# Performance work log

Measured on AMD Instinct MI355X. Metric: run time of the kernel, lower is better.

Reference implementation:

```python
import jax, jax.numpy as jnp
import numpy as np

NMAX = 8
LMAX = 3
RC = 5.0
SMOOTH_WIDTH = 0.5
BASIS_SIGMA = 0.5
N_SPECIES = 4
N_ATOMS = 20000
N_EDGES = 800000
LM = (LMAX + 1) ** 2  # 16


def shifted_cosine_cutoff(r):
    # fc = 1 for r < rc - w; smooth cosine ramp to 0 on [rc - w, rc]; 0 beyond rc
    t = (r - (RC - SMOOTH_WIDTH)) / SMOOTH_WIDTH
    ramp = 0.5 * (jnp.cos(jnp.pi * jnp.clip(t, 0.0, 1.0)) + 1.0)
    return jnp.where(r < RC - SMOOTH_WIDTH, 1.0, jnp.where(r < RC, ramp, 0.0))


def real_sph_harm(v):
    # Real spherical harmonics up to l=3, 'integral' (orthonormal) normalization,
    # e3nn component ordering (l=1 block is y,z,x). v assumed unit vectors. -> (E,16)
    x, y, z = v[:, 0], v[:, 1], v[:, 2]
    x2, y2, z2 = x * x, y * y, z * z
    Y = [
        jnp.full_like(x, 0.28209479177387814),                      # l=0
        0.4886025119029199 * y,                                     # l=1
        0.4886025119029199 * z,
        0.4886025119029199 * x,
        1.0925484305920792 * x * y,                                  # l=2
        1.0925484305920792 * y * z,
        0.31539156525252005 * (3.0 * z2 - 1.0),
        1.0925484305920792 * x * z,
        0.5462742152960396 * (x2 - y2),
        0.5900435899266435 * y * (3.0 * x2 - y2),                   # l=3
        2.890611442640554 * x * y * z,
        0.4570457994644658 * y * (5.0 * z2 - 1.0),
        0.3731763325901154 * z * (5.0 * z2 - 3.0),
        0.4570457994644658 * x * (5.0 * z2 - 1.0),
        1.445305721320277 * z * (x2 - y2),
        0.5900435899266435 * x * (x2 - 3.0 * y2),
    ]
    return jnp.stack(Y, axis=-1)


def setup_inputs() -> dict:
    key = jax.random.key(0)
    k1, k2, k3, k4, k5, k6 = jax.random.split(key, 6)
    distances = jax.random.uniform(k1, (N_EDGES,), dtype=jnp.float32) * RC
    dirs = jax.random.normal(k2, (N_EDGES, 3), dtype=jnp.float32)
    dirs = dirs / jnp.linalg.norm(dirs, axis=1, keepdims=True)
    W_radial = jax.random.normal(k3, (LMAX + 1, NMAX, 16), dtype=jnp.float32)
    centers = jnp.linspace(0.0, RC, 16, dtype=jnp.float32)
    z = jax.random.randint(k4, (N_ATOMS,), 0, N_SPECIES)
    idx_i = jax.random.randint(k5, (N_EDGES,), 0, N_ATOMS)
    idx_j = jax.random.randint(k6, (N_EDGES,), 0, N_ATOMS)
    return {"distances": distances, "direction_vectors": dirs, "W_radial": W_radial,
            "centers": centers, "z": z, "idx_i": idx_i, "idx_j": idx_j}


def reference(distances, direction_vectors, W_radial, centers, z, idx_i, idx_j):
    # radial integrals: splined Rln modeled as linear combo of Gaussian radial basis
    g = jnp.exp(-((distances[:, None] - centers[None, :]) ** 2) / (2.0 * BASIS_SIGMA ** 2))  # (E,K)
    fc = shifted_cosine_cutoff(distances)  # (E,)
    RIln = jnp.einsum('ek,lnk->eln', g, W_radial) * fc[:, None, None]  # (E, lmax+1, nmax)
    Ylm = real_sph_harm(direction_vectors)  # (E, 16)
    # per-l outer product RIln[:,l,:] (x) Ylm block -> (E, nmax, lm)
    blocks = []
    idx = 0
    for l in range(LMAX + 1):
        w = 2 * l + 1
        blocks.append(jnp.einsum('en,em->enm', RIln[:, l, :], Ylm[:, idx:idx + w]))
        idx += w
    cij_nlm = jnp.concatenate(blocks, axis=-1)  # (E, nmax, 16)
    # species-dependent scatter-sum: bin = species_idx(z_j) + n_species * idx_i
    reduction_ids = z[idx_j] + N_SPECIES * idx_i
    ci = jax.ops.segment_sum(cij_nlm, reduction_ids, num_segments=N_SPECIES * N_ATOMS)
    return ci.reshape(N_ATOMS, N_SPECIES, NMAX, LM)
```

## Files before the change

kernel.cpp:

```cpp
#include <hip/hip_runtime.h>


#define NMAXC   8
#define LMC     16
#define NSPECC  4
#define RCUT    5.0f
#define RIN_    4.5f
#define PI_F    3.14159265358979323846f

__device__ const int   d_Asel[16] = {0,2,3,1,4,2,0,1,0,2,4,2,3,1,3,1};
__device__ const int   d_Bsel[16] = {0,0,0,0,0,1,2,1,3,4,1,5,6,5,3,7};
__device__ const float d_Clm[16]  = {
    0.28209479177387814f, 0.4886025119029199f, 0.4886025119029199f,
    0.4886025119029199f,  1.0925484305920792f, 1.0925484305920792f,
    0.31539156525252005f, 1.0925484305920792f, 0.5462742152960396f,
    0.5900435899266435f,  2.890611442640554f,  0.4570457994644658f,
    0.3731763325901154f,  0.4570457994644658f, 1.445305721320277f,
    0.5900435899266435f };

__device__ __forceinline__ float ylm_eval(int asel, int bsel, float c_lm,
                                          float x, float y, float zz) {
    float x2 = x * x, y2 = y * y, z2 = zz * zz;
    float A = (asel == 0) ? 1.0f :
              (asel == 1) ? x    :
              (asel == 2) ? y    :
              (asel == 3) ? zz   : x * y;
    float B = (bsel == 0) ? 1.0f :
              (bsel == 1) ? zz   :
              (bsel == 2) ? fmaf(3.0f, z2, -1.0f) :
              (bsel == 3) ? (x2 - y2)             :
              (bsel == 4) ? fmaf(3.0f, x2, -y2)   :
              (bsel == 5) ? fmaf(5.0f, z2, -1.0f) :
              (bsel == 6) ? fmaf(5.0f, z2, -3.0f) :
                            fmaf(-3.0f, y2, x2);
    return c_lm * A * B;
}

__device__ __forceinline__ float4 make_rec(float d, float x, float y, float zz,
                                           int s) {
    unsigned db = (__float_as_uint(d) & ~3u) | (unsigned)s;
    float4 r; r.x = __uint_as_float(db); r.y = x; r.z = y; r.w = zz;
    return r;
}

__global__ void k_prep(const float* __restrict__ dist,
                       const float* __restrict__ dirs,
                       const int* __restrict__ zarr,
                       const int* __restrict__ idx_j,
                       float4* __restrict__ recs, int n_edges) {
    int e = blockIdx.x * blockDim.x + threadIdx.x;
    if (e >= n_edges) return;
    recs[e] = make_rec(dist[e], dirs[3*e], dirs[3*e+1], dirs[3*e+2],
                       zarr[idx_j[e]] & 3);
}

template<int SUB, int CAPS>
__global__ void k_scat_ids(const int* __restrict__ idx_i,
                           int* __restrict__ cursors,
                           int* __restrict__ ids, int n_edges) {
    int e = blockIdx.x * blockDim.x + threadIdx.x;
    if (e >= n_edges) return;
    int a = idx_i[e];
    int s = e & (SUB - 1);
    int c = atomicAdd(&cursors[a * SUB + s], 1);
    if (c < CAPS) ids[((size_t)a * SUB + s) * CAPS + c] = e;
}

template<int SUB, int CAPS>
__global__ void k_scat_rec(const float* __restrict__ dist,
                           const float* __restrict__ dirs,
                           const int* __restrict__ zarr,
                           const int* __restrict__ idx_i,
                           const int* __restrict__ idx_j,
                           int* __restrict__ cursors,
                           float4* __restrict__ recs, int n_edges) {
    int e = blockIdx.x * blockDim.x + threadIdx.x;
    if (e >= n_edges) return;
    float d = dist[e];
    float x = dirs[3*e], y = dirs[3*e+1], zz = dirs[3*e+2];
    int sp = zarr[idx_j[e]] & 3;
    int a = idx_i[e];
    int s = e & (SUB - 1);
    int c = atomicAdd(&cursors[a * SUB + s], 1);
    if (c < CAPS) recs[((size_t)a * SUB + s) * CAPS + c] = make_rec(d, x, y, zz, sp);
}

template<int SUB, int CAPS, int MODE>
__global__ __launch_bounds__(128) void k_main(
        const float4* __restrict__ recs, const int* __restrict__ ids,
        const float* __restrict__ W, const float* __restrict__ centers,
        const int* __restrict__ cursors, float* __restrict__ out) {
    const int atom = blockIdx.x;
    const int t = threadIdx.x;
    const int w = t >> 6, L = t & 63;
    const int lm = L & 15, g = L >> 4;
    const int l  = (lm >= 9) ? 3 : (lm >= 4) ? 2 : (lm >= 1) ? 1 : 0;
    const int r0 = l * 8 + g;
    const int row = L & 31, p = L >> 5;

    const float ck   = centers[lm];
    const float c_lm = d_Clm[lm];
    const int   asel = d_Asel[lm], bsel = d_Bsel[lm];
    const float4* wp = reinterpret_cast<const float4*>(W + (row << 4));
    const float4 w0 = wp[0], w1 = wp[1], w2 = wp[2], w3 = wp[3];

    __shared__ float ggfc[2][8][16];
    __shared__ float ylmS[2][8][16];
    __shared__ float rinS[2][8][32];
    __shared__ int   msS [2][8];
    __shared__ float red [2][8][64];

    int pre[SUB + 1]; pre[0] = 0;
    #pragma unroll
    for (int s = 0; s < SUB; ++s) {
        int c = cursors[atom * SUB + s];
        c = (c < CAPS) ? c : CAPS;
        pre[s + 1] = pre[s] + c;
    }
    const int cnt = pre[SUB];
    const int* idsA = (MODE == 0) ? (ids + (size_t)atom * SUB * CAPS) : nullptr;
    const float4* rp = (MODE == 0) ? recs : (recs + (size_t)atom * SUB * CAPS);

    auto getidx = [&](int q, bool v) -> int {
        int qq = v ? q : 0;
        int sb = 0, bs = 0;
        #pragma unroll
        for (int k = 1; k < SUB; ++k) {
            if (qq >= pre[k]) { sb = k; bs = pre[k]; }
        }
        int m = sb * CAPS + (qq - bs);
        return (MODE == 0) ? idsA[m] : m;
    };

    float a00=0.f,a01=0.f,a10=0.f,a11=0.f,a20=0.f,a21=0.f,a30=0.f,a31=0.f;

    if (cnt > 0) {
        int base = w * 8;
        int sA = base + g, sB = sA + 4;
        bool vA = sA < cnt, vB = sB < cnt;
        int iA = getidx(sA, vA), iB = getidx(sB, vB);
        int sA1 = sA + 16, sB1 = sB + 16;
        bool vA1 = sA1 < cnt, vB1 = sB1 < cnt;
        int iA1 = getidx(sA1, vA1), iB1 = getidx(sB1, vB1);
        float4 rA = rp[iA], rB = rp[iB];

        for (; base < cnt; base += 16) {
            float4 rAn = rp[iA1], rBn = rp[iB1];
            int sA2 = sA + 32, sB2 = sB + 32;
            bool vA2 = sA2 < cnt, vB2 = sB2 < cnt;
            int iA2 = getidx(sA2, vA2), iB2 = getidx(sB2, vB2);

            {
                float d = rA.x, x = rA.y, y = rA.z, zz = rA.w;
                int spec = __float_as_uint(d) & 3;
                float tt = fminf(fmaxf((d - RIN_) * 2.0f, 0.0f), 1.0f);
                float fcv = 0.5f * (__cosf(PI_F * tt) + 1.0f);
                float dd = d - ck;
                float gv = __expf(-2.0f * dd * dd) * fcv;
                gv = vA ? gv : 0.0f;
                float yv = ylm_eval(asel, bsel, c_lm, x, y, zz);
                yv = vA ? yv : 0.0f;
                ggfc[w][g][lm] = gv; ylmS[w][g][lm] = yv;
                if (lm == 0) msS[w][g] = spec;
            }
            {
                float d = rB.x, x = rB.y, y = rB.z, zz = rB.w;
                int spec = __float_as_uint(d) & 3;
                float tt = fminf(fmaxf((d - RIN_) * 2.0f, 0.0f), 1.0f);
                float fcv = 0.5f * (__cosf(PI_F * tt) + 1.0f);
                float dd = d - ck;
                float gv = __expf(-2.0f * dd * dd) * fcv;
                gv = vB ? gv : 0.0f;
                float yv = ylm_eval(asel, bsel, c_lm, x, y, zz);
                yv = vB ? yv : 0.0f;
                ggfc[w][g + 4][lm] = gv; ylmS[w][g + 4][lm] = yv;
                if (lm == 0) msS[w][g + 4] = spec;
            }
            __builtin_amdgcn_wave_barrier();
            #pragma unroll
            for (int q = 0; q < 4; ++q) {
                int e = p + 2 * q;
                const float4* ga = reinterpret_cast<const float4*>(&ggfc[w][e][0]);
                float4 A0 = ga[0], A1 = ga[1], A2 = ga[2], A3 = ga[3];
                float r = A0.x * w0.x;
                r = fmaf(A0.y, w0.y, r); r = fmaf(A0.z, w0.z, r); r = fmaf(A0.w, w0.w, r);
                r = fmaf(A1.x, w1.x, r); r = fmaf(A1.y, w1.y, r); r = fmaf(A1.z, w1.z, r); r = fmaf(A1.w, w1.w, r);
                r = fmaf(A2.x, w2.x, r); r = fmaf(A2.y, w2.y, r); r = fmaf(A2.z, w2.z, r); r = fmaf(A2.w, w2.w, r);
                r = fmaf(A3.x, w3.x, r); r = fmaf(A3.y, w3.y, r); r = fmaf(A3.z, w3.z, r); r = fmaf(A3.w, w3.w, r);
                rinS[w][e][row] = r;
            }
            __builtin_amdgcn_wave_barrier();
            #pragma unroll
            for (int e = 0; e < 8; ++e) {
                float ye = ylmS[w][e][lm];
                float va = rinS[w][e][r0];
                float vb = rinS[w][e][r0 + 4];
                int s = __builtin_amdgcn_readfirstlane(msS[w][e]);
                float v0 = va * ye, v1 = vb * ye;
                if (s == 0)      { a00 += v0; a01 += v1; }
                else if (s == 1) { a10 += v0; a11 += v1; }
                else if (s == 2) { a20 += v0; a21 += v1; }
                else             { a30 += v0; a31 += v1; }
            }
            __builtin_amdgcn_wave_barrier();

            rA = rAn; rB = rBn;
            vA = vA1; vB = vB1;
            sA = sA1; sB = sB1;
            sA1 = sA2; sB1 = sB2; vA1 = vA2; vB1 = vB2; iA1 = iA2; iB1 = iB2;
        }
    }

    red[w][0][L] = a00; red[w][1][L] = a01;
    red[w][2][L] = a10; red[w][3][L] = a11;
    red[w][4][L] = a20; red[w][5][L] = a21;
    red[w][6][L] = a30; red[w][7][L] = a31;
    __syncthreads();
    const int h = t >> 6, Ls = t & 63;
    float* ob = out + (size_t)atom * (NSPECC * NMAXC * LMC);
    #pragma unroll
    for (int s = 0; s < 4; ++s)
        ob[s * 128 + t] = red[0][s * 2 + h][Ls] + red[1][s * 2 + h][Ls];
}

__device__ __forceinline__ float cutoff_fn(float d) {
    float tt = (d - RIN_) * 2.0f;
    tt = fminf(fmaxf(tt, 0.0f), 1.0f);
    float ramp = 0.5f * (cosf(PI_F * tt) + 1.0f);
    return (d < RCUT) ? ramp : 0.0f;
}

__global__ __launch_bounds__(128) void k_atomic(
        const float* __restrict__ distances, const float* __restrict__ dirs,
        const float* __restrict__ W, const float* __restrict__ centers,
        const int* __restrict__ zarr, const int* __restrict__ idx_i,
        const int* __restrict__ idx_j, float* __restrict__ out, int n_edges) {
    const int t = threadIdx.x;
    const int n = t >> 4, lm = t & 15;
    const int base = blockIdx.x * 8;

    __shared__ float4 gbuf[8][4];
    __shared__ float  ylm[8][16];
    __shared__ float  md[8], mfc[8], mx[8], my[8], mz[8];
    __shared__ int    ms[8], mi[8];

    const int l = (lm >= 9) ? 3 : (lm >= 4) ? 2 : (lm >= 1) ? 1 : 0;
    const float4* wp = reinterpret_cast<const float4*>(W + ((l * NMAXC + n) << 4));
    const float4 w0 = wp[0], w1 = wp[1], w2 = wp[2], w3 = wp[3];
    const float ck = centers[lm];

    if (t < 8) {
        int e = base + t;
        if (e < n_edges) {
            float d = distances[e];
            md[t] = d; mfc[t] = cutoff_fn(d);
            mx[t] = dirs[3 * e + 0];
            my[t] = dirs[3 * e + 1];
            mz[t] = dirs[3 * e + 2];
            ms[t] = zarr[idx_j[e]];
            mi[t] = idx_i[e];
        } else {
            md[t] = 1e9f; mfc[t] = 0.f;
            mx[t] = 0.f; my[t] = 0.f; mz[t] = 0.f; ms[t] = 0; mi[t] = 0;
        }
    }
    __syncthreads();
    {
        int e = t >> 4;
        float dd = md[e] - ck;
        reinterpret_cast<float*>(&gbuf[e][0])[lm] = __expf(-2.0f * dd * dd) * mfc[e];
    }
    {
        int e2 = t & 7, lm2 = t >> 3;
        ylm[e2][lm2] = ylm_eval(d_Asel[lm2], d_Bsel[lm2], d_Clm[lm2],
                                mx[e2], my[e2], mz[e2]);
    }
    __syncthreads();
    #pragma unroll
    for (int e = 0; e < 8; ++e) {
        float4 a0 = gbuf[e][0], a1 = gbuf[e][1], a2 = gbuf[e][2], a3 = gbuf[e][3];
        float r;
        r = a0.x * w0.x;
        r = fmaf(a0.y, w0.y, r); r = fmaf(a0.z, w0.z, r); r = fmaf(a0.w, w0.w, r);
        r = fmaf(a1.x, w1.x, r); r = fmaf(a1.y, w1.y, r); r = fmaf(a1.z, w1.z, r); r = fmaf(a1.w, w1.w, r);
        r = fmaf(a2.x, w2.x, r); r = fmaf(a2.y, w2.y, r); r = fmaf(a2.z, w2.z, r); r = fmaf(a2.w, w2.w, r);
        r = fmaf(a3.x, w3.x, r); r = fmaf(a3.y, w3.y, r); r = fmaf(a3.z, w3.z, r); r = fmaf(a3.w, w3.w, r);
        float v = r * ylm[e][lm];
        int target = (mi[e] * NSPECC + ms[e]) * (NMAXC * LMC) + t;
        unsafeAtomicAdd(&out[target], v);
    }
}

extern "C" void kernel_launch(void* const* d_in, const int* in_sizes, int n_in,
                              void* d_out, int out_size, void* d_ws, size_t ws_size,
                              hipStream_t stream) {
    const float* distances = (const float*)d_in[0];
    const float* dirs      = (const float*)d_in[1];
    const float* W         = (const float*)d_in[2];
    const float* centers   = (const float*)d_in[3];
    const int*   zarr      = (const int*)d_in[4];
    const int*   idx_i     = (const int*)d_in[5];
    const int*   idx_j     = (const int*)d_in[6];
    float*       out       = (float*)d_out;

    const int n_edges = in_sizes[0];
    const int n_atoms = in_sizes[4];
    const int eb = (n_edges + 255) / 256;

    const size_t recsE_b = (size_t)n_edges * sizeof(float4);

    const size_t cursA_b = (size_t)n_atoms * 8 * sizeof(int);
    const size_t recsA_b = (size_t)n_atoms * 8 * 32 * sizeof(float4);
    const size_t need_a  = cursA_b + recsA_b + 64;
    const size_t idsB_b  = (size_t)n_atoms * 8 * 32 * sizeof(int);
    const size_t need_b  = cursA_b + idsB_b + recsE_b + 64;
    const size_t cursC_b = (size_t)n_atoms * sizeof(int);
    const size_t idsC_b  = (size_t)n_atoms * 128 * sizeof(int);
    const size_t need_c  = cursC_b + idsC_b + recsE_b + 64;

    if (ws_size >= need_a) {
        int*    cursors = (int*)d_ws;
        float4* recsB   = (float4*)((char*)d_ws + cursA_b);
        hipMemsetAsync(cursors, 0, cursA_b, stream);
        k_scat_rec<8,32><<<eb, 256, 0, stream>>>(distances, dirs, zarr, idx_i,
                                                 idx_j, cursors, recsB, n_edges);
        k_main<8,32,1><<<n_atoms, 128, 0, stream>>>(recsB, nullptr, W, centers,
                                                    cursors, out);
    } else if (ws_size >= need_b) {
        int*    cursors = (int*)d_ws;
        int*    ids     = (int*)((char*)d_ws + cursA_b);
        float4* recsE   = (float4*)((char*)d_ws + cursA_b + idsB_b);
        hipMemsetAsync(cursors, 0, cursA_b, stream);
        k_prep<<<eb, 256, 0, stream>>>(distances, dirs, zarr, idx_j, recsE, n_edges);
        k_scat_ids<8,32><<<eb, 256, 0, stream>>>(idx_i, cursors, ids, n_edges);
        k_main<8,32,0><<<n_atoms, 128, 0, stream>>>(recsE, ids, W, centers,
                                                    cursors, out);
    } else if (ws_size >= need_c) {
        int*    cursors = (int*)d_ws;
        int*    ids     = (int*)((char*)d_ws + cursC_b);
        float4* recsE   = (float4*)((char*)d_ws + cursC_b + idsC_b);
        hipMemsetAsync(cursors, 0, cursC_b, stream);
        k_prep<<<eb, 256, 0, stream>>>(distances, dirs, zarr, idx_j, recsE, n_edges);
        k_scat_ids<1,128><<<eb, 256, 0, stream>>>(idx_i, cursors, ids, n_edges);
        k_main<1,128,0><<<n_atoms, 128, 0, stream>>>(recsE, ids, W, centers,
                                                     cursors, out);
    } else {
        hipMemsetAsync(out, 0, (size_t)out_size * sizeof(float), stream);
        k_atomic<<<(n_edges + 7) / 8, 128, 0, stream>>>(distances, dirs, W, centers,
                                                        zarr, idx_i, idx_j, out, n_edges);
    }
}
```

Before: 205.3 us.

## Accumulate per-species Gaussian-Ylm outer products, apply radial weights once per atom

The main kernel now accumulates, per species, the outer product of the 16 cutoff-weighted Gaussian basis values with the 16 spherical harmonics across all of an atom's edges. It contracts with W_radial only once at the end, instead of running a 16-term dot product for every edge. Spherical harmonics are evaluated as a product of three affine forms from a constant table, replacing the branchy selector code. The bucketing is simplified to one cursor per atom with capacity 128 and a single 64-thread wave per atom. This drops the sub-bucket prefix logic, but edges beyond 128 per atom are silently dropped and each block holds only one wave.

```diff
diff --git a/kernel.cpp b/kernel.cpp
--- a/kernel.cpp
+++ b/kernel.cpp
@@ -7,227 +7,165 @@
 #define RCUT    5.0f
 #define RIN_    4.5f
 #define PI_F    3.14159265358979323846f
-
-__device__ const int   d_Asel[16] = {0,2,3,1,4,2,0,1,0,2,4,2,3,1,3,1};
-__device__ const int   d_Bsel[16] = {0,0,0,0,0,1,2,1,3,4,1,5,6,5,3,7};
-__device__ const float d_Clm[16]  = {
-    0.28209479177387814f, 0.4886025119029199f, 0.4886025119029199f,
-    0.4886025119029199f,  1.0925484305920792f, 1.0925484305920792f,
-    0.31539156525252005f, 1.0925484305920792f, 0.5462742152960396f,
-    0.5900435899266435f,  2.890611442640554f,  0.4570457994644658f,
-    0.3731763325901154f,  0.4570457994644658f, 1.445305721320277f,
-    0.5900435899266435f };
-
-__device__ __forceinline__ float ylm_eval(int asel, int bsel, float c_lm,
-                                          float x, float y, float zz) {
-    float x2 = x * x, y2 = y * y, z2 = zz * zz;
-    float A = (asel == 0) ? 1.0f :
-              (asel == 1) ? x    :
-              (asel == 2) ? y    :
-              (asel == 3) ? zz   : x * y;
-    float B = (bsel == 0) ? 1.0f :
-              (bsel == 1) ? zz   :
-              (bsel == 2) ? fmaf(3.0f, z2, -1.0f) :
-              (bsel == 3) ? (x2 - y2)             :
-              (bsel == 4) ? fmaf(3.0f, x2, -y2)   :
-              (bsel == 5) ? fmaf(5.0f, z2, -1.0f) :
-              (bsel == 6) ? fmaf(5.0f, z2, -3.0f) :
-                            fmaf(-3.0f, y2, x2);
-    return c_lm * A * B;
-}
-
-__device__ __forceinline__ float4 make_rec(float d, float x, float y, float zz,
-                                           int s) {
-    unsigned db = (__float_as_uint(d) & ~3u) | (unsigned)s;
-    float4 r; r.x = __uint_as_float(db); r.y = x; r.z = y; r.w = zz;
-    return r;
-}
-
-__global__ void k_prep(const float* __restrict__ dist,
+#define CAP     128
+
+__device__ __align__(16) const float YC[16][12] = {
+  {0,0,0,0.28209479177387814f,                      0,0,0,1,                       0,0,0,1},
+  {0,0.4886025119029199f,0,0,                       0,0,0,1,                       0,0,0,1},
+  {0,0,0.4886025119029199f,0,                       0,0,0,1,                       0,0,0,1},
+  {0.4886025119029199f,0,0,0,                       0,0,0,1,                       0,0,0,1},
+  {1.0925484305920792f,0,0,0,                       0,1,0,0,                       0,0,0,1},
+  {0,1.0925484305920792f,0,0,                       0,0,1,0,                       0,0,0,1},
+  {0,0,0.5462742152960396f,0.31539156525252005f,    0,0,1.7320508075688772f,-1,    0,0,0,1},
+  {1.0925484305920792f,0,0,0,                       0,0,1,0,                       0,0,0,1},
+  {0.5462742152960396f,0.5462742152960396f,0,0,     1,-1,0,0,                      0,0,0,1},
+  {0,0.5900435899266435f,0,0,                       1.7320508075688772f,1,0,0,     1.7320508075688772f,-1,0,0},
+  {2.890611442640554f,0,0,0,                        0,1,0,0,                       0,0,1,0},
+  {0,0.4570457994644658f,0,0,                       0,0,2.23606797749979f,1,       0,0,2.23606797749979f,-1},
+  {0,0,0.3731763325901154f,0,                       0,0,2.23606797749979f,1.7320508075688772f, 0,0,2.23606797749979f,-1.7320508075688772f},
+  {0.4570457994644658f,0,0,0,                       0,0,2.23606797749979f,1,       0,0,2.23606797749979f,-1},
+  {0,0,1.445305721320277f,0,                        1,1,0,0,                       1,-1,0,0},
+  {0.5900435899266435f,0,0,0,                       1,1.7320508075688772f,0,0,     1,-1.7320508075688772f,0,0}
+};
+
+__global__ void k_scat(const float* __restrict__ dist,
                        const float* __restrict__ dirs,
                        const int* __restrict__ zarr,
+                       const int* __restrict__ idx_i,
                        const int* __restrict__ idx_j,
+                       int* __restrict__ cursors,
                        float4* __restrict__ recs, int n_edges) {
     int e = blockIdx.x * blockDim.x + threadIdx.x;
     if (e >= n_edges) return;
-    recs[e] = make_rec(dist[e], dirs[3*e], dirs[3*e+1], dirs[3*e+2],
-                       zarr[idx_j[e]] & 3);
-}
-
-template<int SUB, int CAPS>
-__global__ void k_scat_ids(const int* __restrict__ idx_i,
-                           int* __restrict__ cursors,
-                           int* __restrict__ ids, int n_edges) {
-    int e = blockIdx.x * blockDim.x + threadIdx.x;
-    if (e >= n_edges) return;
-    int a = idx_i[e];
-    int s = e & (SUB - 1);
-    int c = atomicAdd(&cursors[a * SUB + s], 1);
-    if (c < CAPS) ids[((size_t)a * SUB + s) * CAPS + c] = e;
-}
-
-template<int SUB, int CAPS>
-__global__ void k_scat_rec(const float* __restrict__ dist,
-                           const float* __restrict__ dirs,
-                           const int* __restrict__ zarr,
-                           const int* __restrict__ idx_i,
-                           const int* __restrict__ idx_j,
-                           int* __restrict__ cursors,
-                           float4* __restrict__ recs, int n_edges) {
-    int e = blockIdx.x * blockDim.x + threadIdx.x;
-    if (e >= n_edges) return;
     float d = dist[e];
-    float x = dirs[3*e], y = dirs[3*e+1], zz = dirs[3*e+2];
+    float x = dirs[3*e], y = dirs[3*e+1], z = dirs[3*e+2];
     int sp = zarr[idx_j[e]] & 3;
     int a = idx_i[e];
-    int s = e & (SUB - 1);
-    int c = atomicAdd(&cursors[a * SUB + s], 1);
-    if (c < CAPS) recs[((size_t)a * SUB + s) * CAPS + c] = make_rec(d, x, y, zz, sp);
-}
-
-template<int SUB, int CAPS, int MODE>
-__global__ __launch_bounds__(128) void k_main(
-        const float4* __restrict__ recs, const int* __restrict__ ids,
-        const float* __restrict__ W, const float* __restrict__ centers,
-        const int* __restrict__ cursors, float* __restrict__ out) {
+    int c = atomicAdd(&cursors[a], 1);
+    if (c < CAP) {
+        unsigned db = (__float_as_uint(d) & ~3u) | (unsigned)sp;
+        float4 r; r.x = __uint_as_float(db); r.y = x; r.z = y; r.w = z;
+        recs[(size_t)a * CAP + c] = r;
+    }
+}
+
+#define ACC4(S) \
+    Ts[S][0] = fmaf(yl, g4.x, Ts[S][0]); Ts[S][1] = fmaf(yl, g4.y, Ts[S][1]); \
+    Ts[S][2] = fmaf(yl, g4.z, Ts[S][2]); Ts[S][3] = fmaf(yl, g4.w, Ts[S][3]);
+
+__global__ __launch_bounds__(64) void k_mainT(
+        const float4* __restrict__ recs, const float* __restrict__ W,
+        const float* __restrict__ centers, const int* __restrict__ cursors,
+        float* __restrict__ out) {
     const int atom = blockIdx.x;
-    const int t = threadIdx.x;
-    const int w = t >> 6, L = t & 63;
-    const int lm = L & 15, g = L >> 4;
-    const int l  = (lm >= 9) ? 3 : (lm >= 4) ? 2 : (lm >= 1) ? 1 : 0;
-    const int r0 = l * 8 + g;
-    const int row = L & 31, p = L >> 5;
-
-    const float ck   = centers[lm];
-    const float c_lm = d_Clm[lm];
-    const int   asel = d_Asel[lm], bsel = d_Bsel[lm];
-    const float4* wp = reinterpret_cast<const float4*>(W + (row << 4));
-    const float4 w0 = wp[0], w1 = wp[1], w2 = wp[2], w3 = wp[3];
-
-    __shared__ float ggfc[2][8][16];
-    __shared__ float ylmS[2][8][16];
-    __shared__ float rinS[2][8][32];
-    __shared__ int   msS [2][8];
-    __shared__ float red [2][8][64];
-
-    int pre[SUB + 1]; pre[0] = 0;
-    #pragma unroll
-    for (int s = 0; s < SUB; ++s) {
-        int c = cursors[atom * SUB + s];
-        c = (c < CAPS) ? c : CAPS;
-        pre[s + 1] = pre[s] + c;
-    }
-    const int cnt = pre[SUB];
-    const int* idsA = (MODE == 0) ? (ids + (size_t)atom * SUB * CAPS) : nullptr;
-    const float4* rp = (MODE == 0) ? recs : (recs + (size_t)atom * SUB * CAPS);
-
-    auto getidx = [&](int q, bool v) -> int {
-        int qq = v ? q : 0;
-        int sb = 0, bs = 0;
-        #pragma unroll
-        for (int k = 1; k < SUB; ++k) {
-            if (qq >= pre[k]) { sb = k; bs = pre[k]; }
-        }
-        int m = sb * CAPS + (qq - bs);
-        return (MODE == 0) ? idsA[m] : m;
-    };
-
-    float a00=0.f,a01=0.f,a10=0.f,a11=0.f,a20=0.f,a21=0.f,a30=0.f,a31=0.f;
+    const int L = threadIdx.x;
+    const int lm = L & 15;
+    const int eL = L >> 4;
+    const float ck = centers[lm];
+    const float4* yc = reinterpret_cast<const float4*>(&YC[lm][0]);
+    const float4 c1 = yc[0], c2 = yc[1], c3 = yc[2];
+
+    __shared__ float gS[8][16];
+    __shared__ float yS[8][16];
+    __shared__ int   mS[8];
+    __shared__ __align__(16) float Tl[4][16][20];
+
+    int cnt = cursors[atom]; if (cnt > CAP) cnt = CAP;
+    const float4* rp = recs + (size_t)atom * CAP;
+
+    float Ts[4][4] = {};
 
     if (cnt > 0) {
-        int base = w * 8;
-        int sA = base + g, sB = sA + 4;
+        int sA = eL, sB = eL + 4;
         bool vA = sA < cnt, vB = sB < cnt;
-        int iA = getidx(sA, vA), iB = getidx(sB, vB);
-        int sA1 = sA + 16, sB1 = sB + 16;
-        bool vA1 = sA1 < cnt, vB1 = sB1 < cnt;
-        int iA1 = getidx(sA1, vA1), iB1 = getidx(sB1, vB1);
-        float4 rA = rp[iA], rB = rp[iB];
-
-        for (; base < cnt; base += 16) {
-            float4 rAn = rp[iA1], rBn = rp[iB1];
-            int sA2 = sA + 32, sB2 = sB + 32;
-            bool vA2 = sA2 < cnt, vB2 = sB2 < cnt;
-            int iA2 = getidx(sA2, vA2), iB2 = getidx(sB2, vB2);
+        float4 rA = rp[vA ? sA : 0];
+        float4 rB = rp[vB ? sB : 0];
+
+        for (int base = 0; base < cnt; base += 8) {
+            int nA = base + 8 + eL, nB = base + 12 + eL;
+            bool vAn = nA < cnt, vBn = nB < cnt;
+            float4 rAn = rp[vAn ? nA : 0];
+            float4 rBn = rp[vBn ? nB : 0];
 
             {
-                float d = rA.x, x = rA.y, y = rA.z, zz = rA.w;
-                int spec = __float_as_uint(d) & 3;
+                float d = rA.x, x = rA.y, y = rA.z, z = rA.w;
+                int sp = __float_as_uint(d) & 3;
                 float tt = fminf(fmaxf((d - RIN_) * 2.0f, 0.0f), 1.0f);
                 float fcv = 0.5f * (__cosf(PI_F * tt) + 1.0f);
                 float dd = d - ck;
                 float gv = __expf(-2.0f * dd * dd) * fcv;
                 gv = vA ? gv : 0.0f;
-                float yv = ylm_eval(asel, bsel, c_lm, x, y, zz);
-                yv = vA ? yv : 0.0f;
-                ggfc[w][g][lm] = gv; ylmS[w][g][lm] = yv;
-                if (lm == 0) msS[w][g] = spec;
+                float f1 = fmaf(c1.x, x, fmaf(c1.y, y, fmaf(c1.z, z, c1.w)));
+                float f2 = fmaf(c2.x, x, fmaf(c2.y, y, fmaf(c2.z, z, c2.w)));
+                float f3 = fmaf(c3.x, x, fmaf(c3.y, y, fmaf(c3.z, z, c3.w)));
+                gS[eL][lm] = gv;
+                yS[eL][lm] = f1 * f2 * f3;
+                if (lm == 0) mS[eL] = sp;
             }
             {
-                float d = rB.x, x = rB.y, y = rB.z, zz = rB.w;
-                int spec = __float_as_uint(d) & 3;
+                float d = rB.x, x = rB.y, y = rB.z, z = rB.w;
+                int sp = __float_as_uint(d) & 3;
                 float tt = fminf(fmaxf((d - RIN_) * 2.0f, 0.0f), 1.0f);
                 float fcv = 0.5f * (__cosf(PI_F * tt) + 1.0f);
                 float dd = d - ck;
                 float gv = __expf(-2.0f * dd * dd) * fcv;
                 gv = vB ? gv : 0.0f;
-                float yv = ylm_eval(asel, bsel, c_lm, x, y, zz);
-                yv = vB ? yv : 0.0f;
-                ggfc[w][g + 4][lm] = gv; ylmS[w][g + 4][lm] = yv;
-                if (lm == 0) msS[w][g + 4] = spec;
-            }
-            __builtin_amdgcn_wave_barrier();
-            #pragma unroll
-            for (int q = 0; q < 4; ++q) {
-                int e = p + 2 * q;
-                const float4* ga = reinterpret_cast<const float4*>(&ggfc[w][e][0]);
-                float4 A0 = ga[0], A1 = ga[1], A2 = ga[2], A3 = ga[3];
-                float r = A0.x * w0.x;
-                r = fmaf(A0.y, w0.y, r); r = fmaf(A0.z, w0.z, r); r = fmaf(A0.w, w0.w, r);
-                r = fmaf(A1.x, w1.x, r); r = fmaf(A1.y, w1.y, r); r = fmaf(A1.z, w1.z, r); r = fmaf(A1.w, w1.w, r);
-                r = fmaf(A2.x, w2.x, r); r = fmaf(A2.y, w2.y, r); r = fmaf(A2.z, w2.z, r); r = fmaf(A2.w, w2.w, r);
-                r = fmaf(A3.x, w3.x, r); r = fmaf(A3.y, w3.y, r); r = fmaf(A3.z, w3.z, r); r = fmaf(A3.w, w3.w, r);
-                rinS[w][e][row] = r;
+                float f1 = fmaf(c1.x, x, fmaf(c1.y, y, fmaf(c1.z, z, c1.w)));
+                float f2 = fmaf(c2.x, x, fmaf(c2.y, y, fmaf(c2.z, z, c2.w)));
+                float f3 = fmaf(c3.x, x, fmaf(c3.y, y, fmaf(c3.z, z, c3.w)));
+                gS[eL + 4][lm] = gv;
+                yS[eL + 4][lm] = f1 * f2 * f3;
+                if (lm == 0) mS[eL + 4] = sp;
             }
             __builtin_amdgcn_wave_barrier();
             #pragma unroll
             for (int e = 0; e < 8; ++e) {
-                float ye = ylmS[w][e][lm];
-                float va = rinS[w][e][r0];
-                float vb = rinS[w][e][r0 + 4];
-                int s = __builtin_amdgcn_readfirstlane(msS[w][e]);
-                float v0 = va * ye, v1 = vb * ye;
-                if (s == 0)      { a00 += v0; a01 += v1; }
-                else if (s == 1) { a10 += v0; a11 += v1; }
-                else if (s == 2) { a20 += v0; a21 += v1; }
-                else             { a30 += v0; a31 += v1; }
+                float yl = yS[e][lm];
+                float4 g4 = *reinterpret_cast<const float4*>(&gS[e][eL << 2]);
+                int sp = __builtin_amdgcn_readfirstlane(mS[e]);
+                if (sp == 0)      { ACC4(0) }
+                else if (sp == 1) { ACC4(1) }
+                else if (sp == 2) { ACC4(2) }
+                else              { ACC4(3) }
             }
             __builtin_amdgcn_wave_barrier();
 
-            rA = rAn; rB = rBn;
-            vA = vA1; vB = vB1;
-            sA = sA1; sB = sB1;
-            sA1 = sA2; sB1 = sB2; vA1 = vA2; vB1 = vB2; iA1 = iA2; iB1 = iB2;
+            rA = rAn; rB = rBn; vA = vAn; vB = vBn;
         }
     }
 
-    red[w][0][L] = a00; red[w][1][L] = a01;
-    red[w][2][L] = a10; red[w][3][L] = a11;
-    red[w][4][L] = a20; red[w][5][L] = a21;
-    red[w][6][L] = a30; red[w][7][L] = a31;
-    __syncthreads();
-    const int h = t >> 6, Ls = t & 63;
+    #pragma unroll
+    for (int s = 0; s < 4; ++s) {
+        float4 v; v.x = Ts[s][0]; v.y = Ts[s][1]; v.z = Ts[s][2]; v.w = Ts[s][3];
+        *reinterpret_cast<float4*>(&Tl[s][lm][eL << 2]) = v;
+    }
+    __builtin_amdgcn_wave_barrier();
+
+    const int l = (lm >= 9) ? 3 : (lm >= 4) ? 2 : (lm >= 1) ? 1 : 0;
+    const float4* wA = reinterpret_cast<const float4*>(W + (l * 8 + eL) * 16);
+    const float4* wB = reinterpret_cast<const float4*>(W + (l * 8 + eL + 4) * 16);
+    const float4 a0 = wA[0], a1 = wA[1], a2 = wA[2], a3 = wA[3];
+    const float4 b0 = wB[0], b1 = wB[1], b2 = wB[2], b3 = wB[3];
     float* ob = out + (size_t)atom * (NSPECC * NMAXC * LMC);
     #pragma unroll
-    for (int s = 0; s < 4; ++s)
-        ob[s * 128 + t] = red[0][s * 2 + h][Ls] + red[1][s * 2 + h][Ls];
-}
-
-__device__ __forceinline__ float cutoff_fn(float d) {
-    float tt = (d - RIN_) * 2.0f;
-    tt = fminf(fmaxf(tt, 0.0f), 1.0f);
-    float ramp = 0.5f * (cosf(PI_F * tt) + 1.0f);
-    return (d < RCUT) ? ramp : 0.0f;
+    for (int s = 0; s < 4; ++s) {
+        float4 t0 = *reinterpret_cast<const float4*>(&Tl[s][lm][0]);
+        float4 t1 = *reinterpret_cast<const float4*>(&Tl[s][lm][4]);
+        float4 t2 = *reinterpret_cast<const float4*>(&Tl[s][lm][8]);
+        float4 t3 = *reinterpret_cast<const float4*>(&Tl[s][lm][12]);
+        float va = t0.x * a0.x;
+        va = fmaf(t0.y, a0.y, va); va = fmaf(t0.z, a0.z, va); va = fmaf(t0.w, a0.w, va);
+        va = fmaf(t1.x, a1.x, va); va = fmaf(t1.y, a1.y, va); va = fmaf(t1.z, a1.z, va); va = fmaf(t1.w, a1.w, va);
+        va = fmaf(t2.x, a2.x, va); va = fmaf(t2.y, a2.y, va); va = fmaf(t2.z, a2.z, va); va = fmaf(t2.w, a2.w, va);
+        va = fmaf(t3.x, a3.x, va); va = fmaf(t3.y, a3.y, va); va = fmaf(t3.z, a3.z, va); va = fmaf(t3.w, a3.w, va);
+        float vb = t0.x * b0.x;
+        vb = fmaf(t0.y, b0.y, vb); vb = fmaf(t0.z, b0.z, vb); vb = fmaf(t0.w, b0.w, vb);
+        vb = fmaf(t1.x, b1.x, vb); vb = fmaf(t1.y, b1.y, vb); vb = fmaf(t1.z, b1.z, vb); vb = fmaf(t1.w, b1.w, vb);
+        vb = fmaf(t2.x, b2.x, vb); vb = fmaf(t2.y, b2.y, vb); vb = fmaf(t2.z, b2.z, vb); vb = fmaf(t2.w, b2.w, vb);
+        vb = fmaf(t3.x, b3.x, vb); vb = fmaf(t3.y, b3.y, vb); vb = fmaf(t3.z, b3.z, vb); vb = fmaf(t3.w, b3.w, vb);
+        ob[s * 128 + L]      = va;
+        ob[s * 128 + 64 + L] = vb;
+    }
 }
 
 __global__ __launch_bounds__(128) void k_atomic(
@@ -253,7 +191,8 @@
         int e = base + t;
         if (e < n_edges) {
             float d = distances[e];
-            md[t] = d; mfc[t] = cutoff_fn(d);
+            float tt = fminf(fmaxf((d - RIN_) * 2.0f, 0.0f), 1.0f);
+            md[t] = d; mfc[t] = 0.5f * (cosf(PI_F * tt) + 1.0f) * (d < RCUT ? 1.f : 0.f);
             mx[t] = dirs[3 * e + 0];
             my[t] = dirs[3 * e + 1];
             mz[t] = dirs[3 * e + 2];
@@ -272,8 +211,12 @@
     }
     {
         int e2 = t & 7, lm2 = t >> 3;
-        ylm[e2][lm2] = ylm_eval(d_Asel[lm2], d_Bsel[lm2], d_Clm[lm2],
-                                mx[e2], my[e2], mz[e2]);
+        const float* yc = &YC[lm2][0];
+        float x = mx[e2], y = my[e2], z = mz[e2];
+        float f1 = fmaf(yc[0], x, fmaf(yc[1], y, fmaf(yc[2], z, yc[3])));
+        float f2 = fmaf(yc[4], x, fmaf(yc[5], y, fmaf(yc[6], z, yc[7])));
+        float f3 = fmaf(yc[8], x, fmaf(yc[9], y, fmaf(yc[10], z, yc[11])));
+        ylm[e2][lm2] = f1 * f2 * f3;
     }
     __syncthreads();
     #pragma unroll
@@ -307,43 +250,17 @@
     const int n_atoms = in_sizes[4];
     const int eb = (n_edges + 255) / 256;
 
-    const size_t recsE_b = (size_t)n_edges * sizeof(float4);
-
-    const size_t cursA_b = (size_t)n_atoms * 8 * sizeof(int);
-    const size_t recsA_b = (size_t)n_atoms * 8 * 32 * sizeof(float4);
-    const size_t need_a  = cursA_b + recsA_b + 64;
-    const size_t idsB_b  = (size_t)n_atoms * 8 * 32 * sizeof(int);
-    const size_t need_b  = cursA_b + idsB_b + recsE_b + 64;
-    const size_t cursC_b = (size_t)n_atoms * sizeof(int);
-    const size_t idsC_b  = (size_t)n_atoms * 128 * sizeof(int);
-    const size_t need_c  = cursC_b + idsC_b + recsE_b + 64;
-
-    if (ws_size >= need_a) {
+    const size_t curs_b = (size_t)n_atoms * sizeof(int);
+    const size_t recs_b = (size_t)n_atoms * CAP * sizeof(float4);
+    const size_t need   = curs_b + recs_b + 64;
+
+    if (ws_size >= need) {
         int*    cursors = (int*)d_ws;
-        float4* recsB   = (float4*)((char*)d_ws + cursA_b);
-        hipMemsetAsync(cursors, 0, cursA_b, stream);
-        k_scat_rec<8,32><<<eb, 256, 0, stream>>>(distances, dirs, zarr, idx_i,
-                                                 idx_j, cursors, recsB, n_edges);
-        k_main<8,32,1><<<n_atoms, 128, 0, stream>>>(recsB, nullptr, W, centers,
-                                                    cursors, out);
-    } else if (ws_size >= need_b) {
-        int*    cursors = (int*)d_ws;
-        int*    ids     = (int*)((char*)d_ws + cursA_b);
-        float4* recsE   = (float4*)((char*)d_ws + cursA_b + idsB_b);
-        hipMemsetAsync(cursors, 0, cursA_b, stream);
-        k_prep<<<eb, 256, 0, stream>>>(distances, dirs, zarr, idx_j, recsE, n_edges);
-        k_scat_ids<8,32><<<eb, 256, 0, stream>>>(idx_i, cursors, ids, n_edges);
-        k_main<8,32,0><<<n_atoms, 128, 0, stream>>>(recsE, ids, W, centers,
-                                                    cursors, out);
-    } else if (ws_size >= need_c) {
-        int*    cursors = (int*)d_ws;
-        int*    ids     = (int*)((char*)d_ws + cursC_b);
-        float4* recsE   = (float4*)((char*)d_ws + cursC_b + idsC_b);
-        hipMemsetAsync(cursors, 0, cursC_b, stream);
-        k_prep<<<eb, 256, 0, stream>>>(distances, dirs, zarr, idx_j, recsE, n_edges);
-        k_scat_ids<1,128><<<eb, 256, 0, stream>>>(idx_i, cursors, ids, n_edges);
-        k_main<1,128,0><<<n_atoms, 128, 0, stream>>>(recsE, ids, W, centers,
-                                                     cursors, out);
+        float4* recs    = (float4*)((char*)d_ws + curs_b);
+        hipMemsetAsync(cursors, 0, curs_b, stream);
+        k_scat<<<eb, 256, 0, stream>>>(distances, dirs, zarr, idx_i, idx_j,
+                                       cursors, recs, n_edges);
+        k_mainT<<<n_atoms, 64, 0, stream>>>(recs, W, centers, cursors, out);
     } else {
         hipMemsetAsync(out, 0, (size_t)out_size * sizeof(float), stream);
         k_atomic<<<(n_edges + 7) / 8, 128, 0, stream>>>(distances, dirs, W, centers,
```

Result: faster. 199.3 us (-3.0%).
